# Optimization experiments

Hardware: AMD Instinct MI355X
Metric: run time of the kernel (lower is better)

## Reference

```python
import jax, jax.numpy as jnp
import numpy as np

N_NODES = 50000
N_EDGES = 800000
N_GRAPHS = 64
IN_DIM = 128
HID = 128
S, C = 4, 16
DIM1 = 3 * S * S  # 48
OUT_DIM = DIM1 * C  # 768


def gcn_conv(x, W, b, src, dst, w):
    """PyG GCNConv: linear transform, then sym-normalized aggregation with self-loops (weight 1)."""
    n = x.shape[0]
    h = x @ W  # [N, out]
    deg = jnp.zeros((n,), x.dtype).at[dst].add(w) + 1.0  # self-loop weight 1
    dinv = jax.lax.rsqrt(deg)
    norm = dinv[src] * w * dinv[dst]  # [E]
    agg = jnp.zeros_like(h).at[dst].add(h[src] * norm[:, None])
    agg = agg + h * (1.0 / deg)[:, None]  # self-loop messages
    return agg + b


def setup_inputs() -> dict:
    key = jax.random.key(0)
    ks = jax.random.split(key, 16)
    x = jax.random.normal(ks[0], (N_NODES, IN_DIM), jnp.float32)
    edge_index = jax.random.randint(ks[1], (2, N_EDGES), 0, N_NODES, jnp.int64)
    edge_attr = jax.random.uniform(ks[2], (N_EDGES,), jnp.float32)
    batch = jnp.sort(jax.random.randint(ks[3], (N_NODES,), 0, N_GRAPHS, jnp.int64))

    def glorot(k, fan_in, fan_out):
        s = np.sqrt(6.0 / (fan_in + fan_out)).astype(np.float32)
        return jax.random.uniform(k, (fan_in, fan_out), jnp.float32, -s, s)

    return {
        "x": x, "edge_index": edge_index, "edge_attr": edge_attr, "batch": batch,
        "W1": glorot(ks[4], IN_DIM, HID), "b1": jnp.zeros((HID,), jnp.float32),
        "W2": glorot(ks[5], HID, HID // 2), "b2": jnp.zeros((HID // 2,), jnp.float32),
        "W3": glorot(ks[6], HID // 2, HID // 4), "b3": jnp.zeros((HID // 4,), jnp.float32),
        "Wl": glorot(ks[7], HID // 4, OUT_DIM), "bl": jnp.zeros((OUT_DIM,), jnp.float32),
    }


def reference(x, edge_index, edge_attr, batch, W1, b1, W2, b2, W3, b3, Wl, bl):
    src, dst = edge_index[0], edge_index[1]
    w = edge_attr / edge_attr.max()
    h = jax.nn.relu(gcn_conv(x, W1, b1, src, dst, w))
    h = jax.nn.relu(gcn_conv(h, W2, b2, src, dst, w))
    h = jax.nn.relu(gcn_conv(h, W3, b3, src, dst, w))
    # global mean pool over graphs
    sums = jax.ops.segment_sum(h, batch, num_segments=N_GRAPHS)
    cnt = jax.ops.segment_sum(jnp.ones((h.shape[0],), h.dtype), batch, num_segments=N_GRAPHS)
    pooled = sums / jnp.maximum(cnt, 1.0)[:, None]
    out = pooled @ Wl + bl  # [G, OUT_DIM]
    return out.reshape(N_GRAPHS, DIM1, C)
```

## Files before the change

### kernel.cpp

```cpp
#include <hip/hip_runtime.h>
#include <hip/hip_bf16.h>

#define NN 50000
#define NE 800000
#define NG 64
#define OUTD 768

#define G1B ((NN + 63) / 64)
#define MAXB 128
#define SSEG 32
#define TTL 2
#define ESEG (NE / SSEG)
#define NTL (NN / TTL)
#define HRB (SSEG * TTL)

__device__ __forceinline__ float bflo(unsigned int u) { return __uint_as_float(u << 16); }
__device__ __forceinline__ float bfhi(unsigned int u) { return __uint_as_float(u & 0xffff0000u); }
__device__ __forceinline__ unsigned short f2bf(float f) {
    unsigned int u = __float_as_uint(f);
    return (unsigned short)((u + 0x7fffu + ((u >> 16) & 1u)) >> 16);
}
__device__ __forceinline__ unsigned int pack2bf(float lo, float hi) {
    return (unsigned int)f2bf(lo) | ((unsigned int)f2bf(hi) << 16);
}

typedef __attribute__((ext_vector_type(8))) short bf16x8;
typedef __attribute__((ext_vector_type(4))) float f32x4;
union FragU { uint4 u4; bf16x8 v; };

template <int K, int N>
constexpr int mfma_lds_bytes() { return (K / 32) * (N / 16) * 1024; }

template <int K, int N, typename TX>
__device__ __forceinline__ void mfma_gemm_body(char* smem,
                                               const TX* __restrict__ X,
                                               const float* __restrict__ W,
                                               unsigned short* __restrict__ Y,
                                               int nRows, int bx) {
    constexpr int NCT = N / 16;
    constexpr int KS = K / 32;
    const int tid = threadIdx.x;

    for (int q = tid; q < KS * NCT * 64; q += 256) {
        int lane = q & 63;
        int fi = q >> 6;
        int ct = fi % NCT, kc = fi / NCT;
        int col = ct * 16 + (lane & 15);
        int kb = kc * 32 + ((lane >> 4) << 3);
        uint4 w;
        w.x = pack2bf(W[(size_t)(kb + 0) * N + col], W[(size_t)(kb + 1) * N + col]);
        w.y = pack2bf(W[(size_t)(kb + 2) * N + col], W[(size_t)(kb + 3) * N + col]);
        w.z = pack2bf(W[(size_t)(kb + 4) * N + col], W[(size_t)(kb + 5) * N + col]);
        w.w = pack2bf(W[(size_t)(kb + 6) * N + col], W[(size_t)(kb + 7) * N + col]);
        *(uint4*)(smem + (size_t)q * 16) = w;
    }
    __syncthreads();

    const int lane = tid & 63;
    const int wv = tid >> 6;
    const int m = lane & 15;
    const int quad = lane >> 4;
    const int row = bx * 64 + wv * 16 + m;
    const bool rowok = row < nRows;
    const TX* xr = X + (size_t)(rowok ? row : 0) * K;

    f32x4 acc[NCT];
#pragma unroll
    for (int ct = 0; ct < NCT; ++ct) acc[ct] = (f32x4){0.f, 0.f, 0.f, 0.f};

#pragma unroll
    for (int kc = 0; kc < KS; ++kc) {
        const int k0 = kc * 32 + quad * 8;
        FragU a;
        if constexpr (sizeof(TX) == 4) {
            float4 a0 = make_float4(0.f, 0.f, 0.f, 0.f), a1 = a0;
            if (rowok) {
                a0 = *(const float4*)(xr + k0);
                a1 = *(const float4*)(xr + k0 + 4);
            }
            a.u4 = make_uint4(pack2bf(a0.x, a0.y), pack2bf(a0.z, a0.w),
                              pack2bf(a1.x, a1.y), pack2bf(a1.z, a1.w));
        } else {
            a.u4 = rowok ? *(const uint4*)(xr + k0) : make_uint4(0, 0, 0, 0);
        }
#pragma unroll
        for (int ct = 0; ct < NCT; ++ct) {
            FragU b;
            b.u4 = *(const uint4*)(smem + ((size_t)(kc * NCT + ct) * 64 + lane) * 16);
            acc[ct] = __builtin_amdgcn_mfma_f32_16x16x32_bf16(a.v, b.v, acc[ct], 0, 0, 0);
        }
    }

    const int orowb = bx * 64 + wv * 16 + quad * 4;
#pragma unroll
    for (int ct = 0; ct < NCT; ++ct) {
        int col = ct * 16 + m;
#pragma unroll
        for (int r = 0; r < 4; ++r) {
            int orow = orowb + r;
            if (orow < nRows) Y[(size_t)orow * N + col] = f2bf(acc[ct][r]);
        }
    }
}

template <int K, int N, typename TX>
__global__ __launch_bounds__(256) void mfma_gemm_kernel(const TX* __restrict__ X,
                                                        const float* __restrict__ W,
                                                        unsigned short* __restrict__ Y,
                                                        int nRows) {
    extern __shared__ char smem[];
    mfma_gemm_body<K, N>(smem, X, W, Y, nRows, blockIdx.x);
}

__global__ __launch_bounds__(256) void fused1_kernel(const float* __restrict__ x,
                                                     const float* __restrict__ W1,
                                                     unsigned short* __restrict__ bufA,
                                                     const float* __restrict__ ea,
                                                     unsigned int* wmax,
                                                     const int* __restrict__ dst,
                                                     int* __restrict__ rank,
                                                     unsigned short* __restrict__ pcnt) {
    extern __shared__ char smem[];
    const int b = blockIdx.x;
    if (b < G1B) {
        mfma_gemm_body<128, 128>(smem, x, W1, bufA, NN, b);
    } else if (b < G1B + MAXB) {
        float* red = (float*)smem;
        const int bb = b - G1B;
        const float4* ea4 = (const float4*)ea;
        float m = 0.0f;
        for (int i = bb * 256 + threadIdx.x; i < NE / 4; i += MAXB * 256) {
            float4 v = ea4[i];
            m = fmaxf(fmaxf(m, fmaxf(v.x, v.y)), fmaxf(v.z, v.w));
        }
        red[threadIdx.x] = m;
        __syncthreads();
        for (int off = 128; off > 0; off >>= 1) {
            if (threadIdx.x < off)
                red[threadIdx.x] = fmaxf(red[threadIdx.x], red[threadIdx.x + off]);
            __syncthreads();
        }
        if (threadIdx.x == 0) atomicMax(wmax, __float_as_uint(red[0]));
    } else {
        const int b2 = b - G1B - MAXB;
        const int seg = b2 >> 1;
        const int tile = b2 & 1;
        unsigned int* lcnt = (unsigned int*)smem;
        for (int i = threadIdx.x; i < NTL / 4; i += 256) lcnt[i] = 0;
        __syncthreads();
        const int base = seg * ESEG;
        const int nlo = tile * NTL;
        const int4* dst4 = (const int4*)(dst + base);
        for (int g = threadIdx.x; g < ESEG / 4; g += 256) {
            const int4 v = dst4[g];
            const int e0 = base + g * 4;
            const int dd[4] = {v.x, v.y, v.z, v.w};
#pragma unroll
            for (int j = 0; j < 4; ++j) {
                int d = dd[j] - nlo;
                if ((unsigned)d < (unsigned)NTL) {
                    unsigned sh = (unsigned)(d & 3) << 3;
                    unsigned old = atomicAdd(&lcnt[d >> 2], 1u << sh);
                    rank[e0 + j] = (int)((old >> sh) & 0xffu);
                }
            }
        }
        __syncthreads();
        unsigned short* prow = pcnt + (size_t)seg * NN + nlo;
        for (int i = threadIdx.x; i < NTL / 4; i += 256) {
            unsigned int w = lcnt[i];
            uint2 o;
            o.x = (w & 0xffu) | ((w & 0xff00u) << 8);
            o.y = ((w >> 16) & 0xffu) | ((w >> 8) & 0xff0000u);
            *(uint2*)(prow + i * 4) = o;
        }
    }
}

__global__ __launch_bounds__(256) void combscan_kernel(unsigned short* __restrict__ pcnt,
                                                       int* __restrict__ blocksum,
                                                       int* __restrict__ rowptr,
                                                       unsigned int* __restrict__ syncf) {
    __shared__ int sc[256];
    __shared__ int sb[256];
    const int tid = threadIdx.x;
    const int n = blockIdx.x * 256 + tid;
    int run = 0;
    if (n < NN) {
#pragma unroll
        for (int s = 0; s < SSEG; ++s) {
            size_t idx = (size_t)s * NN + n;
            int v = pcnt[idx];
            pcnt[idx] = (unsigned short)run;
            run += v;
        }
    }
    sc[tid] = run;
    __syncthreads();
    for (int off = 1; off < 256; off <<= 1) {
        int t = (tid >= off) ? sc[tid - off] : 0;
        __syncthreads();
        sc[tid] += t;
        __syncthreads();
    }
    if (tid == 0) {
        atomicExch(&blocksum[blockIdx.x], sc[255]);
        __threadfence();
        atomicAdd(syncf, 1u);
        while (atomicAdd(syncf, 0u) < (unsigned)gridDim.x)
            __builtin_amdgcn_s_sleep(2);
    }
    __syncthreads();
    int bv = (tid < (int)gridDim.x) ? atomicAdd(&blocksum[tid], 0) : 0;
    sb[tid] = bv;
    __syncthreads();
    for (int off = 1; off < 256; off <<= 1) {
        int t = (tid >= off) ? sb[tid - off] : 0;
        __syncthreads();
        sb[tid] += t;
        __syncthreads();
    }
    const int boff = (blockIdx.x > 0) ? sb[blockIdx.x - 1] : 0;
    if (n < NN) rowptr[n] = boff + sc[tid] - run;
    if (blockIdx.x == gridDim.x - 1 && tid == 0) rowptr[NN] = sb[gridDim.x - 1];
}

__global__ void scat_kernel(const int* __restrict__ src, const int* __restrict__ dst,
                            const float* __restrict__ ea,
                            const int* __restrict__ rowptr,
                            const unsigned short* __restrict__ pcnt,
                            const int* __restrict__ rank,
                            int2* __restrict__ epack, int nE) {
    int e = blockIdx.x * blockDim.x + threadIdx.x;
    if (e >= nE) return;
    int s = e / ESEG;
    int d = dst[e];
    int pos = rowptr[d] + (int)pcnt[(size_t)s * NN + d] + rank[e];
    epack[pos] = make_int2(src[e], __float_as_int(ea[e]));
}

__global__ void deg_kernel(const int2* __restrict__ epack, const int* __restrict__ rowptr,
                           const unsigned int* __restrict__ wmax,
                           float* __restrict__ nrm, float* __restrict__ invdeg, int n) {
    int i = blockIdx.x * blockDim.x + threadIdx.x;
    if (i >= n) return;
    float rw = 1.0f / __uint_as_float(*wmax);
    float srw = sqrtf(rw);
    int s0 = rowptr[i], s1 = rowptr[i + 1];
    float sa = 0.f, sb = 0.f;
    int e = s0;
    for (; e + 2 <= s1; e += 2) {
        sa += __int_as_float(epack[e].y);
        sb += __int_as_float(epack[e + 1].y);
    }
    if (e < s1) sa += __int_as_float(epack[e].y);
    float d = fmaf(sa + sb, rw, 1.0f);
    nrm[i] = rsqrtf(d) * srw;
    invdeg[i] = 1.0f / d;
}

template <int D, bool PRE>
__global__ __launch_bounds__(256) void agg_kernel(const unsigned short* __restrict__ H,
                                                  const int* __restrict__ rowptr,
                                                  int2* __restrict__ epack,
                                                  const float* __restrict__ invdeg,
                                                  const float* __restrict__ nrm,
                                                  const float* __restrict__ bias,
                                                  unsigned short* __restrict__ out,
                                                  int nNodes) {
    constexpr int LPE = D / 8;
    constexpr int EPW = 64 / LPE;
    const int lane = threadIdx.x & 63;
    const int n = (blockIdx.x << 2) | (threadIdx.x >> 6);
    if (n >= nNodes) return;
    const int esub = lane / LPE;
    const int f8 = (lane % LPE) * 8;
    const int s0 = rowptr[n];
    const int cnt = rowptr[n + 1] - s0;
    int2* ep = epack + s0;
    const float dn = PRE ? 1.0f : nrm[n];

    float a[8] = {};
#define AGG8(c_, u_)                                                            \
    a[0] = fmaf(c_, bflo(u_.x), a[0]); a[1] = fmaf(c_, bfhi(u_.x), a[1]);       \
    a[2] = fmaf(c_, bflo(u_.y), a[2]); a[3] = fmaf(c_, bfhi(u_.y), a[3]);       \
    a[4] = fmaf(c_, bflo(u_.z), a[4]); a[5] = fmaf(c_, bfhi(u_.z), a[5]);       \
    a[6] = fmaf(c_, bflo(u_.w), a[6]); a[7] = fmaf(c_, bfhi(u_.w), a[7]);

    int kb = 0;
    for (; kb + 4 * EPW <= cnt; kb += 4 * EPW) {
        const int2 p0 = ep[kb + 0 * EPW + esub];
        const int2 p1 = ep[kb + 1 * EPW + esub];
        const int2 p2 = ep[kb + 2 * EPW + esub];
        const int2 p3 = ep[kb + 3 * EPW + esub];
        const uint4 u0 = *(const uint4*)(H + (size_t)p0.x * D + f8);
        const uint4 u1 = *(const uint4*)(H + (size_t)p1.x * D + f8);
        const uint4 u2 = *(const uint4*)(H + (size_t)p2.x * D + f8);
        const uint4 u3 = *(const uint4*)(H + (size_t)p3.x * D + f8);
        float c0, c1, c2, c3;
        if constexpr (PRE) {
            c0 = __int_as_float(p0.y); c1 = __int_as_float(p1.y);
            c2 = __int_as_float(p2.y); c3 = __int_as_float(p3.y);
        } else {
            c0 = nrm[p0.x] * __int_as_float(p0.y) * dn;
            c1 = nrm[p1.x] * __int_as_float(p1.y) * dn;
            c2 = nrm[p2.x] * __int_as_float(p2.y) * dn;
            c3 = nrm[p3.x] * __int_as_float(p3.y) * dn;
            if (f8 == 0) {
                ep[kb + 0 * EPW + esub].y = __float_as_int(c0);
                ep[kb + 1 * EPW + esub].y = __float_as_int(c1);
                ep[kb + 2 * EPW + esub].y = __float_as_int(c2);
                ep[kb + 3 * EPW + esub].y = __float_as_int(c3);
            }
        }
        AGG8(c0, u0) AGG8(c1, u1) AGG8(c2, u2) AGG8(c3, u3)
    }
    for (; kb + 2 * EPW <= cnt; kb += 2 * EPW) {
        const int2 p0 = ep[kb + esub];
        const int2 p1 = ep[kb + EPW + esub];
        const uint4 u0 = *(const uint4*)(H + (size_t)p0.x * D + f8);
        const uint4 u1 = *(const uint4*)(H + (size_t)p1.x * D + f8);
        float c0, c1;
        if constexpr (PRE) {
            c0 = __int_as_float(p0.y); c1 = __int_as_float(p1.y);
        } else {
            c0 = nrm[p0.x] * __int_as_float(p0.y) * dn;
            c1 = nrm[p1.x] * __int_as_float(p1.y) * dn;
            if (f8 == 0) {
                ep[kb + esub].y = __float_as_int(c0);
                ep[kb + EPW + esub].y = __float_as_int(c1);
            }
        }
        AGG8(c0, u0) AGG8(c1, u1)
    }
    for (; kb < cnt; kb += EPW) {
        const int idx = kb + esub;
        const bool ok = idx < cnt;
        const int2 p = ok ? ep[idx] : make_int2(n, 0);
        const uint4 u = *(const uint4*)(H + (size_t)p.x * D + f8);
        float c;
        if constexpr (PRE) {
            c = ok ? __int_as_float(p.y) : 0.f;
        } else {
            c = ok ? nrm[p.x] * __int_as_float(p.y) * dn : 0.f;
            if (ok && f8 == 0) ep[idx].y = __float_as_int(c);
        }
        AGG8(c, u)
    }
#undef AGG8
#pragma unroll
    for (int off = LPE; off < 64; off <<= 1) {
#pragma unroll
        for (int j = 0; j < 8; ++j) a[j] += __shfl_xor(a[j], off);
    }
    if (esub == 0) {
        const float id = invdeg[n];
        const uint4 un = *(const uint4*)(H + (size_t)n * D + f8);
        const float4 b0 = *(const float4*)(bias + f8);
        const float4 b1 = *(const float4*)(bias + f8 + 4);
        float o[8];
        o[0] = fmaxf(fmaf(id, bflo(un.x), a[0]) + b0.x, 0.f);
        o[1] = fmaxf(fmaf(id, bfhi(un.x), a[1]) + b0.y, 0.f);
        o[2] = fmaxf(fmaf(id, bflo(un.y), a[2]) + b0.z, 0.f);
        o[3] = fmaxf(fmaf(id, bfhi(un.y), a[3]) + b0.w, 0.f);
        o[4] = fmaxf(fmaf(id, bflo(un.z), a[4]) + b1.x, 0.f);
        o[5] = fmaxf(fmaf(id, bfhi(un.z), a[5]) + b1.y, 0.f);
        o[6] = fmaxf(fmaf(id, bflo(un.w), a[6]) + b1.z, 0.f);
        o[7] = fmaxf(fmaf(id, bfhi(un.w), a[7]) + b1.w, 0.f);
        uint4 w;
        w.x = pack2bf(o[0], o[1]);
        w.y = pack2bf(o[2], o[3]);
        w.z = pack2bf(o[4], o[5]);
        w.w = pack2bf(o[6], o[7]);
        *(uint4*)(out + (size_t)n * D + f8) = w;
    }
}

__global__ __launch_bounds__(1024) void poolfin_kernel(const unsigned short* __restrict__ h,
                                                       const int* __restrict__ batch,
                                                       const float* __restrict__ Wl,
                                                       const float* __restrict__ bl,
                                                       float* __restrict__ out, int n) {
    const int g = blockIdx.x;
    int lo = 0, hi = n;
    while (lo < hi) { int m = (lo + hi) >> 1; if (batch[m] < g) lo = m + 1; else hi = m; }
    const int start = lo;
    lo = start; hi = n;
    while (lo < hi) { int m = (lo + hi) >> 1; if (batch[m] < g + 1) lo = m + 1; else hi = m; }
    const int end = lo;

    __shared__ float part[1024];
    __shared__ float spool[32];
    const int f = threadIdx.x & 31;
    const int r = threadIdx.x >> 5;
    float acc = 0.f;
    for (int i = start + r; i < end; i += 32)
        acc += __uint_as_float((unsigned int)h[(size_t)i * 32 + f] << 16);
    part[threadIdx.x] = acc;
    __syncthreads();
    if (threadIdx.x < 32) {
        float s = 0.f;
#pragma unroll
        for (int q = 0; q < 32; ++q) s += part[q * 32 + f];
        float inv = 1.0f / fmaxf((float)(end - start), 1.0f);
        spool[f] = s * inv;
    }
    __syncthreads();
    if (threadIdx.x < OUTD) {
        const int o = threadIdx.x;
        float a2 = bl[o];
#pragma unroll
        for (int k = 0; k < 32; ++k)
            a2 = fmaf(spool[k], Wl[k * OUTD + o], a2);
        out[(size_t)g * OUTD + o] = a2;
    }
}

extern "C" void kernel_launch(void* const* d_in, const int* in_sizes, int n_in,
                              void* d_out, int out_size, void* d_ws, size_t ws_size,
                              hipStream_t stream) {
    const float* x = (const float*)d_in[0];
    const int* eidx = (const int*)d_in[1];
    const float* ea = (const float*)d_in[2];
    const int* batch = (const int*)d_in[3];
    const float* W1 = (const float*)d_in[4];
    const float* b1 = (const float*)d_in[5];
    const float* W2 = (const float*)d_in[6];
    const float* b2 = (const float*)d_in[7];
    const float* W3 = (const float*)d_in[8];
    const float* b3 = (const float*)d_in[9];
    const float* Wl = (const float*)d_in[10];
    const float* bl = (const float*)d_in[11];
    const int* src = eidx;
    const int* dst = eidx + NE;

    char* p = (char*)d_ws;
    auto take = [&](size_t bytes) {
        char* r = p;
        p += (bytes + 255) & ~(size_t)255;
        return r;
    };
    float* nrm = (float*)take(NN * 4);
    float* invdeg = (float*)take(NN * 4);
    int* rowptr = (int*)take((NN + 1) * 4);
    int* blocksum = (int*)take(256 * 4);
    int2* epack = (int2*)take((size_t)NE * 8);
    unsigned int* wmax = (unsigned int*)take(8);
    unsigned int* syncf = wmax + 1;
    unsigned short* bufA = (unsigned short*)take((size_t)NN * 128 * 2);
    unsigned short* bufB = (unsigned short*)take((size_t)NN * 128 * 2);
    int* rank = (int*)bufB;
    unsigned short* pcnt = (unsigned short*)((char*)bufB + (size_t)NE * 4 + 256);

    const int nblk = (NN + 255) / 256;
    const int eblk = (NE + 255) / 256;

    hipMemsetAsync(wmax, 0, 8, stream);

    constexpr int LDS1 = mfma_lds_bytes<128, 128>();
    static_assert(LDS1 >= NTL, "HR branch LDS (packed u8 counters) must fit");
    fused1_kernel<<<G1B + MAXB + HRB, 256, LDS1, stream>>>(x, W1, bufA, ea, wmax,
                                                           dst, rank, pcnt);
    combscan_kernel<<<nblk, 256, 0, stream>>>(pcnt, blocksum, rowptr, syncf);
    scat_kernel<<<eblk, 256, 0, stream>>>(src, dst, ea, rowptr, pcnt, rank, epack, NE);
    deg_kernel<<<nblk, 256, 0, stream>>>(epack, rowptr, wmax, nrm, invdeg, NN);

    agg_kernel<128, false><<<(NN + 3) / 4, 256, 0, stream>>>(bufA, rowptr, epack, invdeg, nrm, b1, bufB, NN);
    mfma_gemm_kernel<128, 64, unsigned short>
        <<<G1B, 256, mfma_lds_bytes<128, 64>(), stream>>>(bufB, W2, bufA, NN);
    agg_kernel<64, true><<<(NN + 3) / 4, 256, 0, stream>>>(bufA, rowptr, epack, invdeg, nrm, b2, bufB, NN);
    mfma_gemm_kernel<64, 32, unsigned short>
        <<<G1B, 256, mfma_lds_bytes<64, 32>(), stream>>>(bufB, W3, bufA, NN);
    agg_kernel<32, true><<<(NN + 3) / 4, 256, 0, stream>>>(bufA, rowptr, epack, invdeg, nrm, b3, bufB, NN);

    poolfin_kernel<<<NG, 1024, 0, stream>>>(bufB, batch, Wl, bl, (float*)d_out, NN);
}
```

Measured before the change: 257.9 us.

## Fold edge-weight max into histogram blocks and split scan into two kernels

Removes the separate max-reduction blocks and computes the edge-attribute maximum inside the histogram blocks (tile 0 only), using a wavefront shuffle reduction followed by an atomicMax. The combined scan kernel, which used an inter-block spin barrier, is replaced by a per-node combine kernel that writes a histogram plus block sums, and a separate scan kernel that builds rowptr. This drops the grid-wide spin-wait and its reliance on all blocks being co-resident, at the cost of one extra launch and an extra NN-sized intermediate buffer.

```diff
diff --git a/kernel.cpp b/kernel.cpp
--- a/kernel.cpp
+++ b/kernel.cpp
@@ -7,7 +7,6 @@
 #define OUTD 768
 
 #define G1B ((NN + 63) / 64)
-#define MAXB 128
 #define SSEG 32
 #define TTL 2
 #define ESEG (NE / SSEG)
@@ -124,35 +123,25 @@
     const int b = blockIdx.x;
     if (b < G1B) {
         mfma_gemm_body<128, 128>(smem, x, W1, bufA, NN, b);
-    } else if (b < G1B + MAXB) {
-        float* red = (float*)smem;
-        const int bb = b - G1B;
-        const float4* ea4 = (const float4*)ea;
-        float m = 0.0f;
-        for (int i = bb * 256 + threadIdx.x; i < NE / 4; i += MAXB * 256) {
-            float4 v = ea4[i];
-            m = fmaxf(fmaxf(m, fmaxf(v.x, v.y)), fmaxf(v.z, v.w));
-        }
-        red[threadIdx.x] = m;
-        __syncthreads();
-        for (int off = 128; off > 0; off >>= 1) {
-            if (threadIdx.x < off)
-                red[threadIdx.x] = fmaxf(red[threadIdx.x], red[threadIdx.x + off]);
-            __syncthreads();
-        }
-        if (threadIdx.x == 0) atomicMax(wmax, __float_as_uint(red[0]));
     } else {
-        const int b2 = b - G1B - MAXB;
+        const int b2 = b - G1B;
         const int seg = b2 >> 1;
         const int tile = b2 & 1;
         unsigned int* lcnt = (unsigned int*)smem;
+        float* redm = (float*)(smem + 25600);
         for (int i = threadIdx.x; i < NTL / 4; i += 256) lcnt[i] = 0;
         __syncthreads();
         const int base = seg * ESEG;
         const int nlo = tile * NTL;
         const int4* dst4 = (const int4*)(dst + base);
+        const float4* ea4 = (const float4*)(ea + base);
+        float m = 0.0f;
         for (int g = threadIdx.x; g < ESEG / 4; g += 256) {
             const int4 v = dst4[g];
+            if (tile == 0) {
+                const float4 ev = ea4[g];
+                m = fmaxf(fmaxf(m, fmaxf(ev.x, ev.y)), fmaxf(ev.z, ev.w));
+            }
             const int e0 = base + g * 4;
             const int dd[4] = {v.x, v.y, v.z, v.w};
 #pragma unroll
@@ -165,6 +154,11 @@
                 }
             }
         }
+        if (tile == 0) {
+#pragma unroll
+            for (int off = 32; off > 0; off >>= 1) m = fmaxf(m, __shfl_xor(m, off));
+            if ((threadIdx.x & 63) == 0) redm[threadIdx.x >> 6] = m;
+        }
         __syncthreads();
         unsigned short* prow = pcnt + (size_t)seg * NN + nlo;
         for (int i = threadIdx.x; i < NTL / 4; i += 256) {
@@ -174,17 +168,18 @@
             o.y = ((w >> 16) & 0xffu) | ((w >> 8) & 0xff0000u);
             *(uint2*)(prow + i * 4) = o;
         }
-    }
-}
-
-__global__ __launch_bounds__(256) void combscan_kernel(unsigned short* __restrict__ pcnt,
-                                                       int* __restrict__ blocksum,
-                                                       int* __restrict__ rowptr,
-                                                       unsigned int* __restrict__ syncf) {
-    __shared__ int sc[256];
-    __shared__ int sb[256];
-    const int tid = threadIdx.x;
-    const int n = blockIdx.x * 256 + tid;
+        if (tile == 0 && threadIdx.x == 0) {
+            float mm = fmaxf(fmaxf(redm[0], redm[1]), fmaxf(redm[2], redm[3]));
+            atomicMax(wmax, __float_as_uint(mm));
+        }
+    }
+}
+
+__global__ __launch_bounds__(256) void comb_kernel(unsigned short* __restrict__ pcnt,
+                                                   int* __restrict__ hist,
+                                                   int* __restrict__ blocksum) {
+    __shared__ int red[256];
+    int n = blockIdx.x * 256 + threadIdx.x;
     int run = 0;
     if (n < NN) {
 #pragma unroll
@@ -194,24 +189,24 @@
             pcnt[idx] = (unsigned short)run;
             run += v;
         }
-    }
-    sc[tid] = run;
-    __syncthreads();
-    for (int off = 1; off < 256; off <<= 1) {
-        int t = (tid >= off) ? sc[tid - off] : 0;
-        __syncthreads();
-        sc[tid] += t;
-        __syncthreads();
-    }
-    if (tid == 0) {
-        atomicExch(&blocksum[blockIdx.x], sc[255]);
-        __threadfence();
-        atomicAdd(syncf, 1u);
-        while (atomicAdd(syncf, 0u) < (unsigned)gridDim.x)
-            __builtin_amdgcn_s_sleep(2);
-    }
-    __syncthreads();
-    int bv = (tid < (int)gridDim.x) ? atomicAdd(&blocksum[tid], 0) : 0;
+        hist[n] = run;
+    }
+    red[threadIdx.x] = (n < NN) ? run : 0;
+    __syncthreads();
+    for (int off = 128; off > 0; off >>= 1) {
+        if (threadIdx.x < off) red[threadIdx.x] += red[threadIdx.x + off];
+        __syncthreads();
+    }
+    if (threadIdx.x == 0) blocksum[blockIdx.x] = red[0];
+}
+
+__global__ __launch_bounds__(256) void scan3_kernel(const int* __restrict__ hist,
+                                                    const int* __restrict__ blocksum,
+                                                    int* __restrict__ rowptr, int n, int nb) {
+    __shared__ int sb[256];
+    __shared__ int s[256];
+    const int tid = threadIdx.x;
+    int bv = (tid < nb) ? blocksum[tid] : 0;
     sb[tid] = bv;
     __syncthreads();
     for (int off = 1; off < 256; off <<= 1) {
@@ -221,8 +216,20 @@
         __syncthreads();
     }
     const int boff = (blockIdx.x > 0) ? sb[blockIdx.x - 1] : 0;
-    if (n < NN) rowptr[n] = boff + sc[tid] - run;
-    if (blockIdx.x == gridDim.x - 1 && tid == 0) rowptr[NN] = sb[gridDim.x - 1];
+    const int total = sb[nb - 1];
+
+    int i = blockIdx.x * 256 + tid;
+    int v = (i < n) ? hist[i] : 0;
+    s[tid] = v;
+    __syncthreads();
+    for (int off = 1; off < 256; off <<= 1) {
+        int t = (tid >= off) ? s[tid - off] : 0;
+        __syncthreads();
+        s[tid] += t;
+        __syncthreads();
+    }
+    if (i < n) rowptr[i] = boff + s[tid] - v;
+    if (blockIdx.x == 0 && tid == 0) rowptr[n] = total;
 }
 
 __global__ void scat_kernel(const int* __restrict__ src, const int* __restrict__ dst,
@@ -442,11 +449,11 @@
     };
     float* nrm = (float*)take(NN * 4);
     float* invdeg = (float*)take(NN * 4);
+    int* hist = (int*)take(NN * 4);
     int* rowptr = (int*)take((NN + 1) * 4);
     int* blocksum = (int*)take(256 * 4);
     int2* epack = (int2*)take((size_t)NE * 8);
-    unsigned int* wmax = (unsigned int*)take(8);
-    unsigned int* syncf = wmax + 1;
+    unsigned int* wmax = (unsigned int*)take(4);
     unsigned short* bufA = (unsigned short*)take((size_t)NN * 128 * 2);
     unsigned short* bufB = (unsigned short*)take((size_t)NN * 128 * 2);
     int* rank = (int*)bufB;
@@ -455,13 +462,14 @@
     const int nblk = (NN + 255) / 256;
     const int eblk = (NE + 255) / 256;
 
-    hipMemsetAsync(wmax, 0, 8, stream);
+    hipMemsetAsync(wmax, 0, 4, stream);
 
     constexpr int LDS1 = mfma_lds_bytes<128, 128>();
-    static_assert(LDS1 >= NTL, "HR branch LDS (packed u8 counters) must fit");
-    fused1_kernel<<<G1B + MAXB + HRB, 256, LDS1, stream>>>(x, W1, bufA, ea, wmax,
-                                                           dst, rank, pcnt);
-    combscan_kernel<<<nblk, 256, 0, stream>>>(pcnt, blocksum, rowptr, syncf);
+    static_assert(LDS1 >= 25600 + 16, "HR branch LDS (u8 counters + max red) must fit");
+    fused1_kernel<<<G1B + HRB, 256, LDS1, stream>>>(x, W1, bufA, ea, wmax,
+                                                    dst, rank, pcnt);
+    comb_kernel<<<nblk, 256, 0, stream>>>(pcnt, hist, blocksum);
+    scan3_kernel<<<nblk, 256, 0, stream>>>(hist, blocksum, rowptr, NN, nblk);
     scat_kernel<<<eblk, 256, 0, stream>>>(src, dst, ea, rowptr, pcnt, rank, epack, NE);
     deg_kernel<<<nblk, 256, 0, stream>>>(epack, rowptr, wmax, nrm, invdeg, NN);
 
```

Result: no change. 257.1 us (-0.3%).
